# Performance work log

Hardware: AMD Instinct MI355X
Metric: run time of the kernel (lower is better)

Reference implementation:

```python
import jax, jax.numpy as jnp
import numpy as np

N_NODES = 100000
N_EDGES = 1600000
IN_FEATS = 128
HID = 128
N_GRAPHS = 1024


def setup_inputs() -> dict:
    key = jax.random.key(0)
    ks = jax.random.split(key, 10)
    h = jax.random.normal(ks[0], (N_NODES, IN_FEATS), dtype=jnp.float32)
    src = jax.random.randint(ks[1], (N_EDGES,), 0, N_NODES)
    dst = jax.random.randint(ks[2], (N_EDGES,), 0, N_NODES)
    graph_ids = jnp.sort(jax.random.randint(ks[3], (N_NODES,), 0, N_GRAPHS))
    # parameters (Glorot-ish scale)
    W1 = jax.random.normal(ks[4], (IN_FEATS, HID), dtype=jnp.float32) / np.sqrt(IN_FEATS)
    b1 = jnp.zeros((HID,), dtype=jnp.float32)
    W2 = jax.random.normal(ks[5], (HID, HID), dtype=jnp.float32) / np.sqrt(HID)
    b2 = jnp.zeros((HID,), dtype=jnp.float32)
    fc_w = jax.random.normal(ks[6], (HID, 1), dtype=jnp.float32) / np.sqrt(HID)
    fc_b = jnp.zeros((1,), dtype=jnp.float32)
    return {"h": h, "src": src, "dst": dst, "graph_ids": graph_ids,
            "n_graphs": N_GRAPHS, "W1": W1, "b1": b1, "W2": W2, "b2": b2,
            "fc_w": fc_w, "fc_b": fc_b}


def _graph_conv(x, W, b, src, dst, c_src, c_dst):
    # DGL GraphConv, norm='both': scale by out_deg^-1/2 at src, aggregate, scale by in_deg^-1/2 at dst
    x = (x * c_src) @ W                      # [N, out]
    agg = jax.ops.segment_sum(x[src], dst, num_segments=x.shape[0])  # SpMM via gather+scatter
    return agg * c_dst + b


def reference(h, src, dst, graph_ids, n_graphs, W1, b1, W2, b2, fc_w, fc_b):
    n = h.shape[0]
    ones_e = jnp.ones(src.shape[0], dtype=h.dtype)
    out_deg = jnp.clip(jax.ops.segment_sum(ones_e, src, num_segments=n), 1.0)
    in_deg = jnp.clip(jax.ops.segment_sum(ones_e, dst, num_segments=n), 1.0)
    c_src = (out_deg ** -0.5)[:, None]
    c_dst = (in_deg ** -0.5)[:, None]

    x = jax.nn.relu(_graph_conv(h, W1, b1, src, dst, c_src, c_dst))
    x = jax.nn.relu(_graph_conv(x, W2, b2, src, dst, c_src, c_dst))

    # dgl.mean_nodes: per-graph mean over nodes
    sums = jax.ops.segment_sum(x, graph_ids, num_segments=n_graphs)        # [G, HID]
    cnts = jnp.clip(jax.ops.segment_sum(jnp.ones((n,), x.dtype), graph_ids,
                                        num_segments=n_graphs), 1.0)
    hg = sums / cnts[:, None]
    return (hg @ fc_w + fc_b).squeeze(-1)    # [G]
```

## Files before the change

kernel.cpp:

```cpp
#include <hip/hip_runtime.h>


#define RANGE 256
#define NBMAX 1024
#define EPB 4096
#define CAP 5120

typedef __attribute__((ext_vector_type(4))) float facc4;
typedef __attribute__((ext_vector_type(8))) short bfrag8;

__device__ inline unsigned short f2bf(float x) {
  unsigned u = __float_as_uint(x);
  u += 0x7FFFu + ((u >> 16) & 1u);
  return (unsigned short)(u >> 16);
}
__device__ inline float bf2f(unsigned short b) {
  return __uint_as_float((unsigned)b << 16);
}
__device__ inline float bflo(unsigned u) { return __uint_as_float(u << 16); }
__device__ inline float bfhi(unsigned u) { return __uint_as_float(u & 0xFFFF0000u); }

__device__ inline void acc8(float* a, const uint4 v) {
  a[0] += bflo(v.x); a[1] += bfhi(v.x);
  a[2] += bflo(v.y); a[3] += bfhi(v.y);
  a[4] += bflo(v.z); a[5] += bfhi(v.z);
  a[6] += bflo(v.w); a[7] += bfhi(v.w);
}

__device__ inline void gather_node(const int* __restrict__ esrc,
                                   const unsigned short* __restrict__ Y,
                                   int beg, int end, int fo, float* acc) {
  int e = beg;
  for (; e < end && (e & 3); ++e) {
    const uint4 v = *(const uint4*)(Y + (size_t)esrc[e] * 128 + fo);
    acc8(acc, v);
  }
  for (; e + 8 <= end; e += 8) {
    const int4 s0 = *(const int4*)(esrc + e);
    const int4 s1 = *(const int4*)(esrc + e + 4);
    const uint4 v0 = *(const uint4*)(Y + (size_t)s0.x * 128 + fo);
    const uint4 v1 = *(const uint4*)(Y + (size_t)s0.y * 128 + fo);
    const uint4 v2 = *(const uint4*)(Y + (size_t)s0.z * 128 + fo);
    const uint4 v3 = *(const uint4*)(Y + (size_t)s0.w * 128 + fo);
    const uint4 v4 = *(const uint4*)(Y + (size_t)s1.x * 128 + fo);
    const uint4 v5 = *(const uint4*)(Y + (size_t)s1.y * 128 + fo);
    const uint4 v6 = *(const uint4*)(Y + (size_t)s1.z * 128 + fo);
    const uint4 v7 = *(const uint4*)(Y + (size_t)s1.w * 128 + fo);
    acc8(acc, v0); acc8(acc, v1); acc8(acc, v2); acc8(acc, v3);
    acc8(acc, v4); acc8(acc, v5); acc8(acc, v6); acc8(acc, v7);
  }
  if (e + 4 <= end) {
    const int4 s0 = *(const int4*)(esrc + e);
    const uint4 v0 = *(const uint4*)(Y + (size_t)s0.x * 128 + fo);
    const uint4 v1 = *(const uint4*)(Y + (size_t)s0.y * 128 + fo);
    const uint4 v2 = *(const uint4*)(Y + (size_t)s0.z * 128 + fo);
    const uint4 v3 = *(const uint4*)(Y + (size_t)s0.w * 128 + fo);
    acc8(acc, v0); acc8(acc, v1); acc8(acc, v2); acc8(acc, v3);
    e += 4;
  }
  for (; e < end; ++e) {
    const uint4 v = *(const uint4*)(Y + (size_t)esrc[e] * 128 + fo);
    acc8(acc, v);
  }
}

__global__ __launch_bounds__(256) void k_part(const int* __restrict__ src,
                                              const int* __restrict__ dst,
                                              int* __restrict__ curS,
                                              int* __restrict__ curD,
                                              unsigned char* __restrict__ outS,
                                              unsigned int* __restrict__ outD,
                                              int E, int NB) {
  __shared__ int hS[NBMAX];
  __shared__ int hD[NBMAX];
  const int t = threadIdx.x;
  for (int i = t; i < NB; i += 256) { hS[i] = 0; hD[i] = 0; }
  __syncthreads();
  const int e0 = blockIdx.x * EPB;
  #pragma unroll
  for (int i = 0; i < EPB / 256; ++i) {
    const int e = e0 + t + 256 * i;
    if (e < E) {
      atomicAdd(&hS[src[e] >> 8], 1);
      atomicAdd(&hD[dst[e] >> 8], 1);
    }
  }
  __syncthreads();
  for (int i = t; i < NB; i += 256) {
    int c = hS[i];
    hS[i] = c ? atomicAdd(&curS[i], c) : 0;
    c = hD[i];
    hD[i] = c ? atomicAdd(&curD[i], c) : 0;
  }
  __syncthreads();
  #pragma unroll
  for (int i = 0; i < EPB / 256; ++i) {
    const int e = e0 + t + 256 * i;
    if (e < E) {
      const int sv = src[e], dv = dst[e];
      int p = atomicAdd(&hS[sv >> 8], 1);
      if (p < CAP) outS[(size_t)(sv >> 8) * CAP + p] = (unsigned char)(sv & 255);
      p = atomicAdd(&hD[dv >> 8], 1);
      if (p < CAP)
        outD[(size_t)(dv >> 8) * CAP + p] =
            ((unsigned)(dv & 255) << 24) | (unsigned)sv;
    }
  }
}

__global__ __launch_bounds__(256) void k_prep(
    const unsigned int* __restrict__ outD, const int* __restrict__ curD,
    int2* __restrict__ rng, int* __restrict__ esrc, float* __restrict__ cD,
    const unsigned char* __restrict__ outS, const int* __restrict__ curS,
    float* __restrict__ cS, const int* __restrict__ gid,
    int* __restrict__ gstart, float* __restrict__ gsum,
    const float* __restrict__ W1, const float* __restrict__ W2,
    unsigned short* __restrict__ Whi, unsigned short* __restrict__ Wlo,
    int N, int NB, int G, int nbN, int nbG) {
  __shared__ int hist[RANGE];
  __shared__ int scn[RANGE];
  const int b = blockIdx.x;
  const int t = threadIdx.x;

  if (b < NB) {
    const int beg = b * CAP;
    const int cnt = min(curD[b], CAP);
    hist[t] = 0;
    __syncthreads();
    for (int e = t; e < cnt; e += 256)
      atomicAdd(&hist[outD[beg + e] >> 24], 1);
    __syncthreads();
    const int deg = hist[t];
    scn[t] = deg;
    __syncthreads();
    #pragma unroll
    for (int o = 1; o < RANGE; o <<= 1) {
      int u = (t >= o) ? scn[t - o] : 0;
      __syncthreads();
      scn[t] += u;
      __syncthreads();
    }
    const int excl = scn[t] - deg;
    const int node = b * RANGE + t;
    if (node < N) {
      cD[node] = rsqrtf((float)(deg > 1 ? deg : 1));
      rng[node] = make_int2(beg + excl, beg + excl + deg);
    }
    scn[t] = excl;
    __syncthreads();
    for (int e = t; e < cnt; e += 256) {
      const unsigned w = outD[beg + e];
      const int pos = beg + atomicAdd(&scn[w >> 24], 1);
      esrc[pos] = (int)(w & 0x1FFFFu);
    }
  } else if (b < 2 * NB) {
    const int bb = b - NB;
    const int beg = bb * CAP;
    const int cnt = min(curS[bb], CAP);
    hist[t] = 0;
    __syncthreads();
    for (int e = t; e < cnt; e += 256)
      atomicAdd(&hist[outS[beg + e]], 1);
    __syncthreads();
    const int node = bb * RANGE + t;
    if (node < N) cS[node] = rsqrtf((float)(hist[t] > 1 ? hist[t] : 1));
  } else if (b < 2 * NB + nbN) {
    const int i = (b - 2 * NB) * 256 + t;
    if (i < N) {
      const int g = gid[i];
      if (i == 0) {
        for (int q = 0; q <= g; ++q) gstart[q] = 0;
      } else {
        const int gp = gid[i - 1];
        for (int q = gp + 1; q <= g; ++q) gstart[q] = i;
      }
      if (i == N - 1) {
        for (int q = g + 1; q <= G; ++q) gstart[q] = N;
      }
    }
  } else if (b < 2 * NB + nbN + nbG) {
    const int i = (b - 2 * NB - nbN) * 256 + t;
    if (i < G) gsum[i] = 0.f;
  } else {
    const int g = (b - 2 * NB - nbN - nbG) * 256 + t;
    const float* W = (g < 16384) ? W1 : W2;
    const int idx = g & 16383;
    const int i = idx & 7;
    const int l = (idx >> 3) & 63;
    const int nb = (idx >> 9) & 7;
    const int kc = idx >> 12;
    const int k = kc * 32 + ((l >> 4) << 3) + i;
    const int n = (nb << 4) + (l & 15);
    const float v = W[k * 128 + n];
    const unsigned short hi = f2bf(v);
    Whi[g] = hi;
    Wlo[g] = f2bf(v - bf2f(hi));
  }
}

__global__ __launch_bounds__(256) void k_mgemm0(const float* __restrict__ Xf,
                                                const unsigned short* __restrict__ Whi,
                                                const unsigned short* __restrict__ Wlo,
                                                const float* __restrict__ cS,
                                                unsigned short* __restrict__ Y,
                                                int N) {
  const int t = threadIdx.x;
  const int wv = t >> 6;
  const int l = t & 63;
  const int lm = l & 15;
  const int lg = l >> 4;
  const int row0 = (blockIdx.x * 4 + wv) * 16;
  const int row = row0 + lm;
  const bool rv = row < N;
  const int rc = rv ? row : 0;
  const float csr = rv ? cS[rc] : 0.f;

  facc4 acc[8];
  #pragma unroll
  for (int nb = 0; nb < 8; ++nb) acc[nb] = (facc4){0.f, 0.f, 0.f, 0.f};

  #pragma unroll
  for (int kc = 0; kc < 4; ++kc) {
    const int k0 = kc * 32 + (lg << 3);
    const float4 x0 = *(const float4*)(Xf + (size_t)rc * 128 + k0);
    const float4 x1 = *(const float4*)(Xf + (size_t)rc * 128 + k0 + 4);
    float a[8] = {x0.x, x0.y, x0.z, x0.w, x1.x, x1.y, x1.z, x1.w};
    #pragma unroll
    for (int i = 0; i < 8; ++i) a[i] *= csr;
    bfrag8 ah, al;
    #pragma unroll
    for (int i = 0; i < 8; ++i) {
      const unsigned short hh = f2bf(a[i]);
      ah[i] = (short)hh;
      al[i] = (short)f2bf(a[i] - bf2f(hh));
    }
    const size_t kb = ((size_t)kc * 8) * 512 + (size_t)l * 8;
    #pragma unroll
    for (int nb = 0; nb < 8; ++nb) {
      const bfrag8 bh = *(const bfrag8*)(Whi + kb + (size_t)nb * 512);
      const bfrag8 bl = *(const bfrag8*)(Wlo + kb + (size_t)nb * 512);
      acc[nb] = __builtin_amdgcn_mfma_f32_16x16x32_bf16(ah, bh, acc[nb], 0, 0, 0);
      acc[nb] = __builtin_amdgcn_mfma_f32_16x16x32_bf16(ah, bl, acc[nb], 0, 0, 0);
      acc[nb] = __builtin_amdgcn_mfma_f32_16x16x32_bf16(al, bh, acc[nb], 0, 0, 0);
    }
  }

  #pragma unroll
  for (int j = 0; j < 4; ++j) {
    const int r = row0 + (lg << 2) + j;
    if (r < N) {
      #pragma unroll
      for (int nb = 0; nb < 8; ++nb)
        Y[(size_t)r * 128 + (nb << 4) + lm] = f2bf(acc[nb][j]);
    }
  }
}

__global__ __launch_bounds__(256) void k_gspmm(
    const int2* __restrict__ rng, const int* __restrict__ esrc,
    const unsigned short* __restrict__ Y1,
    const unsigned short* __restrict__ Whi,
    const unsigned short* __restrict__ Wlo,
    const float* __restrict__ cS, const float* __restrict__ cD,
    const float* __restrict__ bias, unsigned short* __restrict__ Y2, int N) {
  __shared__ unsigned short As[64 * 128];
  const int t = threadIdx.x;
  const int base = blockIdx.x * 64;

  {
    const int lane = t & 15;
    const int grp = t >> 4;
    const int fo = lane * 8;
    #pragma unroll
    for (int s = 0; s < 4; ++s) {
      const int nl = s * 16 + grp;
      const int node = base + nl;
      float acc[8] = {0.f, 0.f, 0.f, 0.f, 0.f, 0.f, 0.f, 0.f};
      if (node < N) {
        const int2 be = rng[node];
        gather_node(esrc, Y1, be.x, be.y, fo, acc);
      }
      uint4 w;
      w.x = (unsigned)f2bf(acc[0]) | ((unsigned)f2bf(acc[1]) << 16);
      w.y = (unsigned)f2bf(acc[2]) | ((unsigned)f2bf(acc[3]) << 16);
      w.z = (unsigned)f2bf(acc[4]) | ((unsigned)f2bf(acc[5]) << 16);
      w.w = (unsigned)f2bf(acc[6]) | ((unsigned)f2bf(acc[7]) << 16);
      *(uint4*)&As[nl * 128 + ((lane ^ (nl & 7)) << 3)] = w;
    }
  }
  __syncthreads();

  const int wv = t >> 6;
  const int l = t & 63;
  const int lm = l & 15;
  const int lg = l >> 4;
  const int row0 = base + wv * 16;
  const int row = row0 + lm;
  const bool rv = row < N;
  const int rc = rv ? row : 0;
  const float csr = rv ? cS[rc] : 0.f;
  const float cdr = rv ? cD[rc] : 0.f;
  const int arow = wv * 16 + lm;

  facc4 acc[8];
  #pragma unroll
  for (int nb = 0; nb < 8; ++nb) acc[nb] = (facc4){0.f, 0.f, 0.f, 0.f};

  #pragma unroll
  for (int kc = 0; kc < 4; ++kc) {
    const int k0 = kc * 32 + (lg << 3);
    const uint4 xb = *(const uint4*)&As[arow * 128 + (((k0 >> 3) ^ (arow & 7)) << 3)];
    float a[8];
    a[0] = bflo(xb.x); a[1] = bfhi(xb.x);
    a[2] = bflo(xb.y); a[3] = bfhi(xb.y);
    a[4] = bflo(xb.z); a[5] = bfhi(xb.z);
    a[6] = bflo(xb.w); a[7] = bfhi(xb.w);
    const float4 b0 = *(const float4*)(bias + k0);
    const float4 b1v = *(const float4*)(bias + k0 + 4);
    const float bb[8] = {b0.x, b0.y, b0.z, b0.w, b1v.x, b1v.y, b1v.z, b1v.w};
    #pragma unroll
    for (int i = 0; i < 8; ++i)
      a[i] = fmaxf(fmaf(a[i], cdr, bb[i]), 0.f) * csr;
    bfrag8 ah, al;
    #pragma unroll
    for (int i = 0; i < 8; ++i) {
      const unsigned short hh = f2bf(a[i]);
      ah[i] = (short)hh;
      al[i] = (short)f2bf(a[i] - bf2f(hh));
    }
    const size_t kb = ((size_t)kc * 8) * 512 + (size_t)l * 8;
    #pragma unroll
    for (int nb = 0; nb < 8; ++nb) {
      const bfrag8 bh = *(const bfrag8*)(Whi + kb + (size_t)nb * 512);
      const bfrag8 bl = *(const bfrag8*)(Wlo + kb + (size_t)nb * 512);
      acc[nb] = __builtin_amdgcn_mfma_f32_16x16x32_bf16(ah, bh, acc[nb], 0, 0, 0);
      acc[nb] = __builtin_amdgcn_mfma_f32_16x16x32_bf16(ah, bl, acc[nb], 0, 0, 0);
      acc[nb] = __builtin_amdgcn_mfma_f32_16x16x32_bf16(al, bh, acc[nb], 0, 0, 0);
    }
  }

  #pragma unroll
  for (int j = 0; j < 4; ++j) {
    const int r = row0 + (lg << 2) + j;
    if (r < N) {
      #pragma unroll
      for (int nb = 0; nb < 8; ++nb)
        Y2[(size_t)r * 128 + (nb << 4) + lm] = f2bf(acc[nb][j]);
    }
  }
}

__global__ __launch_bounds__(256) void k_spmm1(const int2* __restrict__ rng,
                                               const int* __restrict__ esrc,
                                               const unsigned short* __restrict__ Y,
                                               const float* __restrict__ cD,
                                               const float* __restrict__ b2,
                                               const float* __restrict__ fcw,
                                               const int* __restrict__ gid,
                                               float* __restrict__ gsum, int N) {
  __shared__ float sVal[16];
  __shared__ int sGid[16];
  const int t = threadIdx.x;
  const int lane = t & 15;
  const int grp = t >> 4;
  const int node = blockIdx.x * 16 + grp;
  const int fo = lane * 8;

  float acc[8] = {0.f, 0.f, 0.f, 0.f, 0.f, 0.f, 0.f, 0.f};
  if (node < N) {
    const int2 be = rng[node];
    gather_node(esrc, Y, be.x, be.y, fo, acc);
  }

  float s = 0.f;
  if (node < N) {
    const float c = cD[node];
    const float4 bA = *(const float4*)(b2 + fo);
    const float4 bB = *(const float4*)(b2 + fo + 4);
    const float4 wA = *(const float4*)(fcw + fo);
    const float4 wB = *(const float4*)(fcw + fo + 4);
    s += fmaxf(fmaf(acc[0], c, bA.x), 0.f) * wA.x;
    s += fmaxf(fmaf(acc[1], c, bA.y), 0.f) * wA.y;
    s += fmaxf(fmaf(acc[2], c, bA.z), 0.f) * wA.z;
    s += fmaxf(fmaf(acc[3], c, bA.w), 0.f) * wA.w;
    s += fmaxf(fmaf(acc[4], c, bB.x), 0.f) * wB.x;
    s += fmaxf(fmaf(acc[5], c, bB.y), 0.f) * wB.y;
    s += fmaxf(fmaf(acc[6], c, bB.z), 0.f) * wB.z;
    s += fmaxf(fmaf(acc[7], c, bB.w), 0.f) * wB.w;
  }
  #pragma unroll
  for (int o = 8; o > 0; o >>= 1) s += __shfl_down(s, o, 16);
  if (lane == 0) {
    sVal[grp] = (node < N) ? s : 0.f;
    sGid[grp] = (node < N) ? gid[node] : -1;
  }
  __syncthreads();
  if (t == 0) {
    int cg = -1;
    float cs = 0.f;
    #pragma unroll
    for (int k = 0; k < 16; ++k) {
      const int g = sGid[k];
      if (g < 0) continue;
      if (g == cg) {
        cs += sVal[k];
      } else {
        if (cg >= 0) atomicAdd(&gsum[cg], cs);
        cg = g;
        cs = sVal[k];
      }
    }
    if (cg >= 0) atomicAdd(&gsum[cg], cs);
  }
}

__global__ __launch_bounds__(256) void k_final(const float* __restrict__ gsum,
                                               const int* __restrict__ gstart,
                                               const float* __restrict__ fcb,
                                               float* __restrict__ out, int G) {
  const int g = blockIdx.x * 256 + threadIdx.x;
  if (g < G) {
    const int cnt = gstart[g + 1] - gstart[g];
    out[g] = gsum[g] / fmaxf((float)cnt, 1.f) + fcb[0];
  }
}

extern "C" void kernel_launch(void* const* d_in, const int* in_sizes, int n_in,
                              void* d_out, int out_size, void* d_ws, size_t ws_size,
                              hipStream_t stream) {
  const float* h   = (const float*)d_in[0];
  const int*   src = (const int*)d_in[1];
  const int*   dst = (const int*)d_in[2];
  const int*   gid = (const int*)d_in[3];
  const float* W1  = (const float*)d_in[5];
  const float* b1  = (const float*)d_in[6];
  const float* W2  = (const float*)d_in[7];
  const float* b2  = (const float*)d_in[8];
  const float* fcw = (const float*)d_in[9];
  const float* fcb = (const float*)d_in[10];
  float* out = (float*)d_out;

  const int N = in_sizes[0] / 128;
  const int E = in_sizes[1];
  const int G = out_size;
  const int NB = (N + RANGE - 1) / RANGE;

  char* base = (char*)d_ws;
  size_t off = 0;
  auto alloc = [&](size_t bytes) -> void* {
    void* p = base + off;
    off += (bytes + 1023) & ~(size_t)1023;
    return p;
  };
  unsigned short* Y1 = (unsigned short*)alloc((size_t)N * 128 * 2);
  unsigned short* Y2 = (unsigned short*)alloc((size_t)N * 128 * 2);
  unsigned int*  outD = (unsigned int*)Y1;
  unsigned char* outS = (unsigned char*)Y1 + (size_t)NB * CAP * 4;
  float* cS     = (float*)alloc((size_t)N * 4);
  float* cD     = (float*)alloc((size_t)N * 4);
  int2*  rng    = (int2*)alloc((size_t)N * 8);
  int*   esrc   = (int*)alloc((size_t)NB * CAP * 4);
  int*   cur    = (int*)alloc((size_t)2 * NBMAX * 4);
  float* gsum   = (float*)alloc((size_t)G * 4);
  int*   gstart = (int*)alloc((size_t)(G + 1) * 4);
  unsigned short* Whi = (unsigned short*)alloc(32768 * 2);
  unsigned short* Wlo = (unsigned short*)alloc(32768 * 2);
  (void)ws_size; (void)n_in;

  hipMemsetAsync(cur, 0, (size_t)2 * NBMAX * 4, stream);

  const int nbP = (E + EPB - 1) / EPB;
  const int nbN = (N + 255) / 256;
  const int nbG = (G + 255) / 256;
  k_part<<<nbP, 256, 0, stream>>>(src, dst, cur, cur + NBMAX, outS, outD, E, NB);
  k_prep<<<2 * NB + nbN + nbG + 128, 256, 0, stream>>>(
      outD, cur + NBMAX, rng, esrc, cD, outS, cur, cS, gid, gstart, gsum,
      W1, W2, Whi, Wlo, N, NB, G, nbN, nbG);

  const int nbM = (N + 63) / 64;
  const int nbS = (N + 15) / 16;
  k_mgemm0<<<nbM, 256, 0, stream>>>(h, Whi, Wlo, cS, Y1, N);
  k_gspmm<<<nbM, 256, 0, stream>>>(rng, esrc, Y1, Whi + 16384, Wlo + 16384,
                                   cS, cD, b1, Y2, N);
  k_spmm1<<<nbS, 256, 0, stream>>>(rng, esrc, Y2, cD, b2, fcw, gid, gsum, N);
  k_final<<<nbG, 256, 0, stream>>>(gsum, gstart, fcb, out, G);
}
```

Baseline: 235.9 us.

## Split fused gather-GEMM into separate SpMM and GEMM kernels; vectorize partition loads

The fused layer-1 kernel, which gathered neighbor rows into shared memory and then ran the MFMA GEMM, is replaced by a standalone gather kernel (16 nodes per block) that writes bf16 aggregates to global memory. A templated GEMM kernel then applies bias, relu and scaling and multiplies by W2. The aim is better occupancy and load balance for the gather, since the fused kernel's 16KB of LDS and its GEMM phase limited parallelism. The cost is an extra round trip of N×128 bf16 through global memory and one more launch. Separately, the edge partition kernel now reads src/dst with int4 loads.

```diff
diff --git a/kernel.cpp b/kernel.cpp
--- a/kernel.cpp
+++ b/kernel.cpp
@@ -78,11 +78,22 @@
   __syncthreads();
   const int e0 = blockIdx.x * EPB;
   #pragma unroll
-  for (int i = 0; i < EPB / 256; ++i) {
-    const int e = e0 + t + 256 * i;
-    if (e < E) {
-      atomicAdd(&hS[src[e] >> 8], 1);
-      atomicAdd(&hD[dst[e] >> 8], 1);
+  for (int i = 0; i < EPB / 1024; ++i) {
+    const int e = e0 + (i * 256 + t) * 4;
+    if (e + 3 < E) {
+      const int4 s4 = *(const int4*)(src + e);
+      const int4 d4 = *(const int4*)(dst + e);
+      atomicAdd(&hS[s4.x >> 8], 1); atomicAdd(&hS[s4.y >> 8], 1);
+      atomicAdd(&hS[s4.z >> 8], 1); atomicAdd(&hS[s4.w >> 8], 1);
+      atomicAdd(&hD[d4.x >> 8], 1); atomicAdd(&hD[d4.y >> 8], 1);
+      atomicAdd(&hD[d4.z >> 8], 1); atomicAdd(&hD[d4.w >> 8], 1);
+    } else {
+      for (int j = 0; j < 4; ++j) {
+        if (e + j < E) {
+          atomicAdd(&hS[src[e + j] >> 8], 1);
+          atomicAdd(&hD[dst[e + j] >> 8], 1);
+        }
+      }
     }
   }
   __syncthreads();
@@ -94,16 +105,36 @@
   }
   __syncthreads();
   #pragma unroll
-  for (int i = 0; i < EPB / 256; ++i) {
-    const int e = e0 + t + 256 * i;
-    if (e < E) {
-      const int sv = src[e], dv = dst[e];
-      int p = atomicAdd(&hS[sv >> 8], 1);
-      if (p < CAP) outS[(size_t)(sv >> 8) * CAP + p] = (unsigned char)(sv & 255);
-      p = atomicAdd(&hD[dv >> 8], 1);
-      if (p < CAP)
-        outD[(size_t)(dv >> 8) * CAP + p] =
-            ((unsigned)(dv & 255) << 24) | (unsigned)sv;
+  for (int i = 0; i < EPB / 1024; ++i) {
+    const int e = e0 + (i * 256 + t) * 4;
+    if (e + 3 < E) {
+      const int4 s4 = *(const int4*)(src + e);
+      const int4 d4 = *(const int4*)(dst + e);
+      const int sv[4] = {s4.x, s4.y, s4.z, s4.w};
+      const int dv[4] = {d4.x, d4.y, d4.z, d4.w};
+      #pragma unroll
+      for (int j = 0; j < 4; ++j) {
+        int p = atomicAdd(&hS[sv[j] >> 8], 1);
+        if (p < CAP)
+          outS[(size_t)(sv[j] >> 8) * CAP + p] = (unsigned char)(sv[j] & 255);
+        p = atomicAdd(&hD[dv[j] >> 8], 1);
+        if (p < CAP)
+          outD[(size_t)(dv[j] >> 8) * CAP + p] =
+              ((unsigned)(dv[j] & 255) << 24) | (unsigned)sv[j];
+      }
+    } else {
+      for (int j = 0; j < 4; ++j) {
+        if (e + j < E) {
+          const int sv = src[e + j], dv = dst[e + j];
+          int p = atomicAdd(&hS[sv >> 8], 1);
+          if (p < CAP)
+            outS[(size_t)(sv >> 8) * CAP + p] = (unsigned char)(sv & 255);
+          p = atomicAdd(&hD[dv >> 8], 1);
+          if (p < CAP)
+            outD[(size_t)(dv >> 8) * CAP + p] =
+                ((unsigned)(dv & 255) << 24) | (unsigned)sv;
+        }
+      }
     }
   }
 }
@@ -198,12 +229,16 @@
   }
 }
 
-__global__ __launch_bounds__(256) void k_mgemm0(const float* __restrict__ Xf,
-                                                const unsigned short* __restrict__ Whi,
-                                                const unsigned short* __restrict__ Wlo,
-                                                const float* __restrict__ cS,
-                                                unsigned short* __restrict__ Y,
-                                                int N) {
+template <int MODE>
+__global__ __launch_bounds__(256) void k_mgemm(const float* __restrict__ Xf,
+                                               const unsigned short* __restrict__ Xb,
+                                               const unsigned short* __restrict__ Whi,
+                                               const unsigned short* __restrict__ Wlo,
+                                               const float* __restrict__ cS,
+                                               const float* __restrict__ cD,
+                                               const float* __restrict__ bias,
+                                               unsigned short* __restrict__ Y,
+                                               int N) {
   const int t = threadIdx.x;
   const int wv = t >> 6;
   const int l = t & 63;
@@ -214,6 +249,7 @@
   const bool rv = row < N;
   const int rc = rv ? row : 0;
   const float csr = rv ? cS[rc] : 0.f;
+  const float cdr = (MODE == 1) ? (rv ? cD[rc] : 0.f) : 0.f;
 
   facc4 acc[8];
   #pragma unroll
@@ -222,11 +258,27 @@
   #pragma unroll
   for (int kc = 0; kc < 4; ++kc) {
     const int k0 = kc * 32 + (lg << 3);
-    const float4 x0 = *(const float4*)(Xf + (size_t)rc * 128 + k0);
-    const float4 x1 = *(const float4*)(Xf + (size_t)rc * 128 + k0 + 4);
-    float a[8] = {x0.x, x0.y, x0.z, x0.w, x1.x, x1.y, x1.z, x1.w};
-    #pragma unroll
-    for (int i = 0; i < 8; ++i) a[i] *= csr;
+    float a[8];
+    if constexpr (MODE == 0) {
+      const float4 x0 = *(const float4*)(Xf + (size_t)rc * 128 + k0);
+      const float4 x1 = *(const float4*)(Xf + (size_t)rc * 128 + k0 + 4);
+      a[0] = x0.x; a[1] = x0.y; a[2] = x0.z; a[3] = x0.w;
+      a[4] = x1.x; a[5] = x1.y; a[6] = x1.z; a[7] = x1.w;
+      #pragma unroll
+      for (int i = 0; i < 8; ++i) a[i] *= csr;
+    } else {
+      const uint4 xb = *(const uint4*)(Xb + (size_t)rc * 128 + k0);
+      a[0] = bflo(xb.x); a[1] = bfhi(xb.x);
+      a[2] = bflo(xb.y); a[3] = bfhi(xb.y);
+      a[4] = bflo(xb.z); a[5] = bfhi(xb.z);
+      a[6] = bflo(xb.w); a[7] = bfhi(xb.w);
+      const float4 b0 = *(const float4*)(bias + k0);
+      const float4 b1 = *(const float4*)(bias + k0 + 4);
+      const float bb[8] = {b0.x, b0.y, b0.z, b0.w, b1.x, b1.y, b1.z, b1.w};
+      #pragma unroll
+      for (int i = 0; i < 8; ++i)
+        a[i] = fmaxf(fmaf(a[i], cdr, bb[i]), 0.f) * csr;
+    }
     bfrag8 ah, al;
     #pragma unroll
     for (int i = 0; i < 8; ++i) {
@@ -256,108 +308,16 @@
   }
 }
 
-__global__ __launch_bounds__(256) void k_gspmm(
-    const int2* __restrict__ rng, const int* __restrict__ esrc,
-    const unsigned short* __restrict__ Y1,
-    const unsigned short* __restrict__ Whi,
-    const unsigned short* __restrict__ Wlo,
-    const float* __restrict__ cS, const float* __restrict__ cD,
-    const float* __restrict__ bias, unsigned short* __restrict__ Y2, int N) {
-  __shared__ unsigned short As[64 * 128];
-  const int t = threadIdx.x;
-  const int base = blockIdx.x * 64;
-
-  {
-    const int lane = t & 15;
-    const int grp = t >> 4;
-    const int fo = lane * 8;
-    #pragma unroll
-    for (int s = 0; s < 4; ++s) {
-      const int nl = s * 16 + grp;
-      const int node = base + nl;
-      float acc[8] = {0.f, 0.f, 0.f, 0.f, 0.f, 0.f, 0.f, 0.f};
-      if (node < N) {
-        const int2 be = rng[node];
-        gather_node(esrc, Y1, be.x, be.y, fo, acc);
-      }
-      uint4 w;
-      w.x = (unsigned)f2bf(acc[0]) | ((unsigned)f2bf(acc[1]) << 16);
-      w.y = (unsigned)f2bf(acc[2]) | ((unsigned)f2bf(acc[3]) << 16);
-      w.z = (unsigned)f2bf(acc[4]) | ((unsigned)f2bf(acc[5]) << 16);
-      w.w = (unsigned)f2bf(acc[6]) | ((unsigned)f2bf(acc[7]) << 16);
-      *(uint4*)&As[nl * 128 + ((lane ^ (nl & 7)) << 3)] = w;
-    }
-  }
-  __syncthreads();
-
-  const int wv = t >> 6;
-  const int l = t & 63;
-  const int lm = l & 15;
-  const int lg = l >> 4;
-  const int row0 = base + wv * 16;
-  const int row = row0 + lm;
-  const bool rv = row < N;
-  const int rc = rv ? row : 0;
-  const float csr = rv ? cS[rc] : 0.f;
-  const float cdr = rv ? cD[rc] : 0.f;
-  const int arow = wv * 16 + lm;
-
-  facc4 acc[8];
-  #pragma unroll
-  for (int nb = 0; nb < 8; ++nb) acc[nb] = (facc4){0.f, 0.f, 0.f, 0.f};
-
-  #pragma unroll
-  for (int kc = 0; kc < 4; ++kc) {
-    const int k0 = kc * 32 + (lg << 3);
-    const uint4 xb = *(const uint4*)&As[arow * 128 + (((k0 >> 3) ^ (arow & 7)) << 3)];
-    float a[8];
-    a[0] = bflo(xb.x); a[1] = bfhi(xb.x);
-    a[2] = bflo(xb.y); a[3] = bfhi(xb.y);
-    a[4] = bflo(xb.z); a[5] = bfhi(xb.z);
-    a[6] = bflo(xb.w); a[7] = bfhi(xb.w);
-    const float4 b0 = *(const float4*)(bias + k0);
-    const float4 b1v = *(const float4*)(bias + k0 + 4);
-    const float bb[8] = {b0.x, b0.y, b0.z, b0.w, b1v.x, b1v.y, b1v.z, b1v.w};
-    #pragma unroll
-    for (int i = 0; i < 8; ++i)
-      a[i] = fmaxf(fmaf(a[i], cdr, bb[i]), 0.f) * csr;
-    bfrag8 ah, al;
-    #pragma unroll
-    for (int i = 0; i < 8; ++i) {
-      const unsigned short hh = f2bf(a[i]);
-      ah[i] = (short)hh;
-      al[i] = (short)f2bf(a[i] - bf2f(hh));
-    }
-    const size_t kb = ((size_t)kc * 8) * 512 + (size_t)l * 8;
-    #pragma unroll
-    for (int nb = 0; nb < 8; ++nb) {
-      const bfrag8 bh = *(const bfrag8*)(Whi + kb + (size_t)nb * 512);
-      const bfrag8 bl = *(const bfrag8*)(Wlo + kb + (size_t)nb * 512);
-      acc[nb] = __builtin_amdgcn_mfma_f32_16x16x32_bf16(ah, bh, acc[nb], 0, 0, 0);
-      acc[nb] = __builtin_amdgcn_mfma_f32_16x16x32_bf16(ah, bl, acc[nb], 0, 0, 0);
-      acc[nb] = __builtin_amdgcn_mfma_f32_16x16x32_bf16(al, bh, acc[nb], 0, 0, 0);
-    }
-  }
-
-  #pragma unroll
-  for (int j = 0; j < 4; ++j) {
-    const int r = row0 + (lg << 2) + j;
-    if (r < N) {
-      #pragma unroll
-      for (int nb = 0; nb < 8; ++nb)
-        Y2[(size_t)r * 128 + (nb << 4) + lm] = f2bf(acc[nb][j]);
-    }
-  }
-}
-
-__global__ __launch_bounds__(256) void k_spmm1(const int2* __restrict__ rng,
-                                               const int* __restrict__ esrc,
-                                               const unsigned short* __restrict__ Y,
-                                               const float* __restrict__ cD,
-                                               const float* __restrict__ b2,
-                                               const float* __restrict__ fcw,
-                                               const int* __restrict__ gid,
-                                               float* __restrict__ gsum, int N) {
+template <int MODE>
+__global__ __launch_bounds__(256) void k_spmm(const int2* __restrict__ rng,
+                                              const int* __restrict__ esrc,
+                                              const unsigned short* __restrict__ Y,
+                                              unsigned short* __restrict__ aggb,
+                                              const float* __restrict__ cD,
+                                              const float* __restrict__ b2,
+                                              const float* __restrict__ fcw,
+                                              const int* __restrict__ gid,
+                                              float* __restrict__ gsum, int N) {
   __shared__ float sVal[16];
   __shared__ int sGid[16];
   const int t = threadIdx.x;
@@ -372,45 +332,56 @@
     gather_node(esrc, Y, be.x, be.y, fo, acc);
   }
 
-  float s = 0.f;
-  if (node < N) {
-    const float c = cD[node];
-    const float4 bA = *(const float4*)(b2 + fo);
-    const float4 bB = *(const float4*)(b2 + fo + 4);
-    const float4 wA = *(const float4*)(fcw + fo);
-    const float4 wB = *(const float4*)(fcw + fo + 4);
-    s += fmaxf(fmaf(acc[0], c, bA.x), 0.f) * wA.x;
-    s += fmaxf(fmaf(acc[1], c, bA.y), 0.f) * wA.y;
-    s += fmaxf(fmaf(acc[2], c, bA.z), 0.f) * wA.z;
-    s += fmaxf(fmaf(acc[3], c, bA.w), 0.f) * wA.w;
-    s += fmaxf(fmaf(acc[4], c, bB.x), 0.f) * wB.x;
-    s += fmaxf(fmaf(acc[5], c, bB.y), 0.f) * wB.y;
-    s += fmaxf(fmaf(acc[6], c, bB.z), 0.f) * wB.z;
-    s += fmaxf(fmaf(acc[7], c, bB.w), 0.f) * wB.w;
-  }
-  #pragma unroll
-  for (int o = 8; o > 0; o >>= 1) s += __shfl_down(s, o, 16);
-  if (lane == 0) {
-    sVal[grp] = (node < N) ? s : 0.f;
-    sGid[grp] = (node < N) ? gid[node] : -1;
-  }
-  __syncthreads();
-  if (t == 0) {
-    int cg = -1;
-    float cs = 0.f;
+  if constexpr (MODE == 0) {
+    if (node < N) {
+      uint4 w;
+      w.x = (unsigned)f2bf(acc[0]) | ((unsigned)f2bf(acc[1]) << 16);
+      w.y = (unsigned)f2bf(acc[2]) | ((unsigned)f2bf(acc[3]) << 16);
+      w.z = (unsigned)f2bf(acc[4]) | ((unsigned)f2bf(acc[5]) << 16);
+      w.w = (unsigned)f2bf(acc[6]) | ((unsigned)f2bf(acc[7]) << 16);
+      *(uint4*)(aggb + (size_t)node * 128 + fo) = w;
+    }
+  } else {
+    float s = 0.f;
+    if (node < N) {
+      const float c = cD[node];
+      const float4 bA = *(const float4*)(b2 + fo);
+      const float4 bB = *(const float4*)(b2 + fo + 4);
+      const float4 wA = *(const float4*)(fcw + fo);
+      const float4 wB = *(const float4*)(fcw + fo + 4);
+      s += fmaxf(fmaf(acc[0], c, bA.x), 0.f) * wA.x;
+      s += fmaxf(fmaf(acc[1], c, bA.y), 0.f) * wA.y;
+      s += fmaxf(fmaf(acc[2], c, bA.z), 0.f) * wA.z;
+      s += fmaxf(fmaf(acc[3], c, bA.w), 0.f) * wA.w;
+      s += fmaxf(fmaf(acc[4], c, bB.x), 0.f) * wB.x;
+      s += fmaxf(fmaf(acc[5], c, bB.y), 0.f) * wB.y;
+      s += fmaxf(fmaf(acc[6], c, bB.z), 0.f) * wB.z;
+      s += fmaxf(fmaf(acc[7], c, bB.w), 0.f) * wB.w;
+    }
     #pragma unroll
-    for (int k = 0; k < 16; ++k) {
-      const int g = sGid[k];
-      if (g < 0) continue;
-      if (g == cg) {
-        cs += sVal[k];
-      } else {
-        if (cg >= 0) atomicAdd(&gsum[cg], cs);
-        cg = g;
-        cs = sVal[k];
-      }
-    }
-    if (cg >= 0) atomicAdd(&gsum[cg], cs);
+    for (int o = 8; o > 0; o >>= 1) s += __shfl_down(s, o, 16);
+    if (lane == 0) {
+      sVal[grp] = (node < N) ? s : 0.f;
+      sGid[grp] = (node < N) ? gid[node] : -1;
+    }
+    __syncthreads();
+    if (t == 0) {
+      int cg = -1;
+      float cs = 0.f;
+      #pragma unroll
+      for (int k = 0; k < 16; ++k) {
+        const int g = sGid[k];
+        if (g < 0) continue;
+        if (g == cg) {
+          cs += sVal[k];
+        } else {
+          if (cg >= 0) atomicAdd(&gsum[cg], cs);
+          cg = g;
+          cs = sVal[k];
+        }
+      }
+      if (cg >= 0) atomicAdd(&gsum[cg], cs);
+    }
   }
 }
 
@@ -452,10 +423,10 @@
     off += (bytes + 1023) & ~(size_t)1023;
     return p;
   };
-  unsigned short* Y1 = (unsigned short*)alloc((size_t)N * 128 * 2);
-  unsigned short* Y2 = (unsigned short*)alloc((size_t)N * 128 * 2);
-  unsigned int*  outD = (unsigned int*)Y1;
-  unsigned char* outS = (unsigned char*)Y1 + (size_t)NB * CAP * 4;
+  unsigned short* Y    = (unsigned short*)alloc((size_t)N * 128 * 2);
+  unsigned short* aggb = (unsigned short*)alloc((size_t)N * 128 * 2);
+  unsigned int*  outD = (unsigned int*)aggb;
+  unsigned char* outS = (unsigned char*)aggb + (size_t)NB * CAP * 4;
   float* cS     = (float*)alloc((size_t)N * 4);
   float* cD     = (float*)alloc((size_t)N * 4);
   int2*  rng    = (int2*)alloc((size_t)N * 8);
@@ -479,9 +450,13 @@
 
   const int nbM = (N + 63) / 64;
   const int nbS = (N + 15) / 16;
-  k_mgemm0<<<nbM, 256, 0, stream>>>(h, Whi, Wlo, cS, Y1, N);
-  k_gspmm<<<nbM, 256, 0, stream>>>(rng, esrc, Y1, Whi + 16384, Wlo + 16384,
-                                   cS, cD, b1, Y2, N);
-  k_spmm1<<<nbS, 256, 0, stream>>>(rng, esrc, Y2, cD, b2, fcw, gid, gsum, N);
+  k_mgemm<0><<<nbM, 256, 0, stream>>>(h, (const unsigned short*)nullptr, Whi,
+                                      Wlo, cS, cD, b1, Y, N);
+  k_spmm<0><<<nbS, 256, 0, stream>>>(rng, esrc, Y, aggb, cD, b2, fcw, gid,
+                                     gsum, N);
+  k_mgemm<1><<<nbM, 256, 0, stream>>>((const float*)nullptr, aggb, Whi + 16384,
+                                      Wlo + 16384, cS, cD, b1, Y, N);
+  k_spmm<1><<<nbS, 256, 0, stream>>>(rng, esrc, Y, aggb, cD, b2, fcw, gid,
+                                     gsum, N);
   k_final<<<nbG, 256, 0, stream>>>(gsum, gstart, fcb, out, G);
 }
```

Result: no change. 231.8 us (-1.7%).
